# Kernel tuning notes

Hardware: AMD Instinct MI355X
Metric: run time of the kernel (lower is better)

## Reference

```python
import jax, jax.numpy as jnp
from jax import lax
import numpy as np

DIM = 256
HEADS = 8
DIM_HEAD = 32          # must equal W (see rearrange constraint in original code)
INNER = HEADS * DIM_HEAD
FF_INNER = DIM * 4
KH = 8                 # height_top_k (selects over dim_head axis due to axis mislabeling)
KW = 8                 # width_top_k  (selects over spatial H axis)
B, H, W = 8, 256, 32
EPS = 1e-5


def setup_inputs() -> dict:
    key = jax.random.key(0)
    ks = jax.random.split(key, 12)
    def rn(k, shape, fan_in):
        return jax.random.normal(k, shape, dtype=jnp.float32) / np.sqrt(fan_in)
    return {
        "x": jax.random.normal(ks[0], (B, DIM, H, W), dtype=jnp.float32),
        "cln_g": jnp.ones((1, DIM, 1, 1), dtype=jnp.float32),
        "cln_b": jnp.zeros((1, DIM, 1, 1), dtype=jnp.float32),
        "w_qkv": rn(ks[1], (INNER * 3, DIM), DIM),
        "w_out": rn(ks[2], (DIM, INNER), INNER),
        "b_out": jnp.zeros((DIM,), dtype=jnp.float32),
        "w_dw": rn(ks[3], (DIM, 1, 3, 3), 9),
        "b_dw": jnp.zeros((DIM,), dtype=jnp.float32),
        "w_comb": rn(ks[4], (DIM, DIM * 2), DIM * 2),
        "b_comb": jnp.zeros((DIM,), dtype=jnp.float32),
        "w_ff1": rn(ks[5], (FF_INNER, DIM), DIM),
        "b_ff1": jnp.zeros((FF_INNER,), dtype=jnp.float32),
        "w_ffdw": rn(ks[6], (FF_INNER, 1, 3, 3), 9),
        "b_ffdw": jnp.zeros((FF_INNER,), dtype=jnp.float32),
        "w_ff2": rn(ks[7], (DIM, FF_INNER), FF_INNER),
        "b_ff2": jnp.zeros((DIM,), dtype=jnp.float32),
    }


def _conv1x1(x, w, b=None):
    y = jnp.einsum('oc,bchw->bohw', w, x)
    return y if b is None else y + b[None, :, None, None]


def _dwconv3(x, w, b):
    y = lax.conv_general_dilated(x, w, (1, 1), 'SAME',
                                 feature_group_count=x.shape[1],
                                 dimension_numbers=('NCHW', 'OIHW', 'NCHW'))
    return y + b[None, :, None, None]


def _inorm(t):
    # nn.InstanceNorm2d(affine=False): normalize per (b, c) over spatial dims
    m = jnp.mean(t, axis=(2, 3), keepdims=True)
    v = jnp.var(t, axis=(2, 3), keepdims=True)
    return (t - m) / jnp.sqrt(v + EPS)


def _l2n(t):
    # F.normalize(dim=-1): here last axis is spatial W (acts as feature 'd')
    return t / jnp.clip(jnp.linalg.norm(t, axis=-1, keepdims=True), 1e-12)


def reference(x, cln_g, cln_b, w_qkv, w_out, b_out, w_dw, b_dw, w_comb, b_comb,
              w_ff1, b_ff1, w_ffdw, b_ffdw, w_ff2, b_ff2):
    b, c, h, w = x.shape
    # ---- DPSA branch ----
    mean = jnp.mean(x, axis=1, keepdims=True)
    var = jnp.var(x, axis=1, keepdims=True)
    xn = (x - mean) / jnp.sqrt(var + EPS) * cln_g + cln_b
    qkv = _conv1x1(xn, w_qkv)
    q, k, v = jnp.split(qkv, 3, axis=1)
    # '(b h) c x y' layout: axes are (b*heads, dim_head, H, W)
    q, k, v = (t.reshape(b * HEADS, DIM_HEAD, h, w) for t in (q, k, v))
    q, k = _l2n(q), _l2n(k)
    q_probe = q.sum(axis=(1, 2))                       # (bh, W)
    # 'height' selection -> actually over dim_head axis (axis 1)
    sh = jnp.einsum('bd,bhd->bh', q_probe, k.sum(axis=2))
    ih = lax.top_k(sh, KH)[1]                          # (bh, KH)
    k = jnp.take_along_axis(k, ih[:, :, None, None], axis=1)
    v = jnp.take_along_axis(v, ih[:, :, None, None], axis=1)
    # 'width' selection -> actually over spatial H axis (axis 2)
    sw = jnp.einsum('bd,bwd->bw', q_probe, k.sum(axis=1))
    iw = lax.top_k(sw, KW)[1]                          # (bh, KW)
    k = jnp.take_along_axis(k, iw[:, None, :, None], axis=2)
    v = jnp.take_along_axis(v, iw[:, None, :, None], axis=2)
    q2 = q.reshape(b * HEADS, DIM_HEAD * h, w)         # (bh, dh*H, W)
    k2 = k.reshape(b * HEADS, KH * KW, w)
    v2 = v.reshape(b * HEADS, KH * KW, w)
    attn = jax.nn.softmax(jnp.einsum('bid,bjd->bij', q2, k2), axis=-1)
    o = jnp.einsum('bij,bjd->bid', attn, v2)           # (bh, dh*H, W); dh == W
    # rearrange '(b h) (x y) d -> b (h d) x y'
    o = o.reshape(b, HEADS, h, w, w).transpose(0, 1, 4, 2, 3).reshape(b, HEADS * w, h, w)
    attn_branch = _conv1x1(o, w_out, b_out)
    # ---- conv branch + combine ----
    conv_branch = _dwconv3(x, w_dw, b_dw)
    comb = _conv1x1(jnp.concatenate([attn_branch, conv_branch], axis=1), w_comb, b_comb) + x
    # ---- feed-forward ----
    h1 = jax.nn.gelu(_inorm(_conv1x1(comb, w_ff1, b_ff1)), approximate=False)
    h2 = h1 + jax.nn.gelu(_inorm(_dwconv3(h1, w_ffdw, b_ffdw)), approximate=False)
    return _inorm(_conv1x1(h2, w_ff2, b_ff2))
```

## Files before the change

### kernel.cpp

```cpp
#include <hip/hip_runtime.h>
#include <hip/hip_fp16.h>
#include <math.h>

#define B_    8
#define CDIM  256
#define HH    256
#define WW    32
#define PP    8192
#define HEADS 8
#define FFI   1024

typedef _Float16 f16;
typedef _Float16 half8 __attribute__((ext_vector_type(8)));
typedef _Float16 half4 __attribute__((ext_vector_type(4)));
typedef _Float16 f16x2v __attribute__((ext_vector_type(2)));
typedef float f32x4 __attribute__((ext_vector_type(4)));

static const size_t OFF_QPROBE = 16908288;
static const size_t OFF_SH     = 16910336;
static const size_t OFF_IH     = 16912384;
static const size_t OFF_IW     = 16912896;
static const size_t OFF_STM    = 16913408;
static const size_t OFF_STR    = 16921600;
static const size_t OFF_VSEL   = 16929792;
static const size_t OFF_W16    = 17060864;

#define WH_QKV  0
#define WH_OUT  196608
#define WH_COMB 262144
#define WH_FF1  393216
#define WH_FF2  655360

__device__ __forceinline__ float gelu_f(float x) {
  float z = fabsf(x) * 0.70710678118f;
  float t = __builtin_amdgcn_rcpf(1.0f + 0.3275911f * z);
  float poly = t * (0.254829592f +
               t * (-0.284496736f +
               t * (1.421413741f +
               t * (-1.453152027f +
               t * 1.061405429f))));
  float e = 1.0f - poly * __expf(-z * z);
  return 0.5f * x * (1.0f + copysignf(e, x));
}

__global__ __launch_bounds__(256) void k_wcvt(const float* __restrict__ s0,
                                              const float* __restrict__ s1,
                                              const float* __restrict__ s2,
                                              const float* __restrict__ s3,
                                              const float* __restrict__ s4,
                                              f16* __restrict__ dst) {
  int blk = blockIdx.x;
  const float* src; size_t base;
  if (blk < 192)      { src = s0; base = WH_QKV;  }
  else if (blk < 256) { src = s1; base = WH_OUT;  blk -= 192; }
  else if (blk < 384) { src = s2; base = WH_COMB; blk -= 256; }
  else if (blk < 640) { src = s3; base = WH_FF1;  blk -= 384; }
  else                { src = s4; base = WH_FF2;  blk -= 640; }
  int off = blk * 1024 + threadIdx.x * 4;
  float4 v = *(const float4*)(src + off);
  half4 h; h[0] = (f16)v.x; h[1] = (f16)v.y; h[2] = (f16)v.z; h[3] = (f16)v.w;
  *(half4*)(dst + base + off) = h;
}

__global__ __launch_bounds__(256) void k_lnxn(const float* __restrict__ x,
                                              const float* __restrict__ g,
                                              const float* __restrict__ bb,
                                              f16* __restrict__ xn) {
  int idx = blockIdx.x * 256 + threadIdx.x;
  int b = idx >> 13, p = idx & 8191;
  const float* xp = x + (size_t)b * CDIM * PP + p;
  float s = 0.f, s2 = 0.f;
  for (int c = 0; c < CDIM; c++) { float v = xp[(size_t)c * PP]; s += v; s2 += v * v; }
  float m = s * (1.0f / CDIM);
  float var = s2 * (1.0f / CDIM) - m * m;
  float r = rsqrtf(var + 1e-5f);
  f16* xo = xn + (size_t)b * CDIM * PP + p;
  for (int c = 0; c < CDIM; c++)
    xo[(size_t)c * PP] = (f16)((xp[(size_t)c * PP] - m) * r * g[c] + bb[c]);
}

#define MF_STAGE                                                                   \
  int t = threadIdx.x;                                                             \
  int nw_ = gridDim.x * gridDim.y;                     \
  int hb_ = blockIdx.x + gridDim.x * blockIdx.y;                                   \
  int wk_ = (hb_ & 7) * (nw_ >> 3) + (hb_ >> 3);                                   \
  int gy_ = gridDim.y;                                      \
  int sh_ = __ffs(gy_) - 1;                                                        \
  int p0 = (wk_ >> sh_) * 128, m0 = (wk_ & (gy_ - 1)) * 128, z = blockIdx.z;       \
  int lane = t & 63, wave = t >> 6;                                                \
  int wm = (wave >> 1) * 64, wp = (wave & 1) * 64;                                 \
  int col = lane & 15, quad = lane >> 4;                                           \
  f32x4 acc[4][4];                                                                 \
  _Pragma("unroll") for (int i = 0; i < 4; i++)                                    \
  _Pragma("unroll") for (int j = 0; j < 4; j++)                                    \
      acc[i][j] = (f32x4){0.f, 0.f, 0.f, 0.f};                                     \
  int am = t >> 1, ak = (t & 1) * 16;                                              \
  int bp = (t & 15) * 8, bk = (t >> 4) * 2;                                        \
  int erot = t & 7;                                                                \
  const f16* wr0 = W + (size_t)(m0 + am) * K + ak;                                 \
  const f16* br0 = inB + (size_t)bk * PP + p0 + bp;                                \
  half8 w0 = *(const half8*)wr0;                                                   \
  half8 w1 = *(const half8*)(wr0 + 8);                                             \
  half8 r0 = *(const half8*)br0;                                                   \
  half8 r1 = *(const half8*)(br0 + PP);                                            \
  for (int k0 = 0; k0 < K; k0 += 32) {                                             \
    *(half8*)&As[am][ak] = w0;                                                     \
    *(half8*)&As[am][ak + 8] = w1;                                                 \
    _Pragma("unroll") for (int e0 = 0; e0 < 8; e0++) {                             \
      int e = (e0 + erot) & 7;                                                     \
      f16x2v pr2; pr2[0] = r0[e]; pr2[1] = r1[e];                                  \
      *(f16x2v*)&Bs[bp + e][bk] = pr2;                                             \
    }                                                                              \
    __syncthreads();                                                               \
    int kn = (k0 + 32 < K) ? k0 + 32 : k0;  \
    w0 = *(const half8*)(wr0 + kn);                                                \
    w1 = *(const half8*)(wr0 + kn + 8);                                            \
    r0 = *(const half8*)(inB + (size_t)(kn + bk) * PP + p0 + bp);                  \
    r1 = *(const half8*)(inB + (size_t)(kn + bk + 1) * PP + p0 + bp);              \
    half8 af[4], bf[4];                                                            \
    _Pragma("unroll") for (int i = 0; i < 4; i++)                                  \
      af[i] = *(const half8*)&As[wm + i * 16 + col][quad * 8];                     \
    _Pragma("unroll") for (int j = 0; j < 4; j++)                                  \
      bf[j] = *(const half8*)&Bs[wp + j * 16 + col][quad * 8];                     \
    _Pragma("unroll") for (int i = 0; i < 4; i++)                                  \
    _Pragma("unroll") for (int j = 0; j < 4; j++)                                  \
        acc[i][j] = __builtin_amdgcn_mfma_f32_16x16x32_f16(af[i], bf[j],           \
                                                           acc[i][j], 0, 0, 0);    \
    __syncthreads();                                                               \
  }

__global__ __launch_bounds__(256) void k_mf(const f16* __restrict__ W,
                                            const f16* __restrict__ In, size_t inZ,
                                            f16* __restrict__ OutH,
                                            float* __restrict__ OutF, size_t outZ,
                                            const float* __restrict__ bias,
                                            const float* __restrict__ resid, size_t residZ,
                                            int K) {
  __shared__ f16 As[128][40];
  __shared__ f16 Bs[128][40];
  const f16* inB = In + (size_t)blockIdx.z * inZ;
  MF_STAGE
#pragma unroll
  for (int i = 0; i < 4; i++) {
    int mb = m0 + wm + i * 16 + quad * 4;
#pragma unroll
    for (int r = 0; r < 4; r++) {
      int m = mb + r;
      float bs = bias ? bias[m] : 0.f;
#pragma unroll
      for (int j = 0; j < 4; j++) {
        int p = p0 + wp + j * 16 + col;
        float v = acc[i][j][r] + bs;
        size_t off = (size_t)z * outZ + (size_t)m * PP + p;
        if (resid) v += resid[(size_t)z * residZ + (size_t)m * PP + p];
        if (OutF) OutF[off] = v;
        else OutH[off] = (f16)v;
      }
    }
  }
}

__global__ __launch_bounds__(256) void k_mf_qk(const f16* __restrict__ W,
                                               const f16* __restrict__ In, size_t inZ,
                                               f16* __restrict__ qkO, int K) {
  __shared__ f16 As[128][40];
  __shared__ f16 Bs[128][40];
  const f16* inB = In + (size_t)blockIdx.z * inZ;
  MF_STAGE
#pragma unroll
  for (int i = 0; i < 4; i++) {
    int mb = m0 + wm + i * 16 + quad * 4;
#pragma unroll
    for (int r = 0; r < 4; r++) {
      int m = mb + r;
      size_t base = (size_t)z * 512 * PP + (size_t)m * PP;
#pragma unroll
      for (int jp = 0; jp < 2; jp++) {
        float a0 = acc[i][2 * jp][r], a1 = acc[i][2 * jp + 1][r];
        float ss = a0 * a0 + a1 * a1;
        ss += __shfl_xor(ss, 1);
        ss += __shfl_xor(ss, 2);
        ss += __shfl_xor(ss, 4);
        ss += __shfl_xor(ss, 8);
        float inv = 1.0f / fmaxf(sqrtf(ss), 1e-12f);
        int pa = p0 + wp + 2 * jp * 16 + col;
        qkO[base + pa] = (f16)(a0 * inv);
        qkO[base + pa + 16] = (f16)(a1 * inv);
      }
    }
  }
}

__global__ __launch_bounds__(256) void k_probe(const f16* __restrict__ qk,
                                               float* __restrict__ qprobe,
                                               float* __restrict__ sh) {
  __shared__ float red[64][32];
  __shared__ float qp[32];
  __shared__ float ksum[32][32];
  int bh = blockIdx.x, b = bh >> 3, hd = bh & 7;
  int t = threadIdx.x;
  const f16* qb = qk + ((size_t)(b * 512 + hd * 32)) * PP;
  {
    int g = t >> 2, wq = (t & 3) * 8;
    float s[8];
#pragma unroll
    for (int e = 0; e < 8; e++) s[e] = 0.f;
    for (int it = 0; it < 128; it++) {
      int row = g * 128 + it;
      half8 v = *(const half8*)(qb + (size_t)(row >> 8) * PP + (row & 255) * 32 + wq);
#pragma unroll
      for (int e = 0; e < 8; e++) s[e] += (float)v[e];
    }
#pragma unroll
    for (int e = 0; e < 8; e++) red[g][wq + e] = s[e];
  }
  __syncthreads();
  if (t < 32) {
    float a = 0.f;
    for (int g = 0; g < 64; g++) a += red[g][t];
    qp[t] = a;
    qprobe[bh * 32 + t] = a;
  }
  const f16* kb = qk + ((size_t)(b * 512 + 256 + hd * 32)) * PP;
  {
    int d = t >> 3, wq = (t & 7) * 4;
    float s[4] = {0.f, 0.f, 0.f, 0.f};
    for (int h = 0; h < 256; h++) {
      half4 v = *(const half4*)(kb + (size_t)d * PP + h * 32 + wq);
#pragma unroll
      for (int e = 0; e < 4; e++) s[e] += (float)v[e];
    }
#pragma unroll
    for (int e = 0; e < 4; e++) ksum[d][wq + e] = s[e];
  }
  __syncthreads();
  if (t < 32) {
    float a = 0.f;
    for (int w = 0; w < 32; w++) a += qp[w] * ksum[t][w];
    sh[bh * 32 + t] = a;
  }
}

__global__ __launch_bounds__(64) void k_topk_h(const float* __restrict__ sh, int* __restrict__ ih) {
  int bh = blockIdx.x;
  if (threadIdx.x != 0) return;
  float v[32];
#pragma unroll
  for (int i = 0; i < 32; i++) v[i] = sh[bh * 32 + i];
  for (int s = 0; s < 8; s++) {
    int bi = 0; float bv = v[0];
#pragma unroll
    for (int i = 1; i < 32; i++) { if (v[i] > bv) { bv = v[i]; bi = i; } }
    ih[bh * 8 + s] = bi;
    v[bi] = -3.4e38f;
  }
}

__global__ __launch_bounds__(256) void k_sw_topk(const f16* __restrict__ qk,
                                                 const float* __restrict__ qprobe,
                                                 const int* __restrict__ ih,
                                                 int* __restrict__ iw) {
  __shared__ float qp[32];
  __shared__ float sw[256];
  __shared__ int ihs[8];
  int bh = blockIdx.x, b = bh >> 3, hd = bh & 7;
  int t = threadIdx.x;
  if (t < 32) qp[t] = qprobe[bh * 32 + t];
  if (t < 8) ihs[t] = ih[bh * 8 + t];
  __syncthreads();
  const f16* kb = qk + ((size_t)(b * 512 + 256 + hd * 32)) * PP;
  float s = 0.f;
  for (int a = 0; a < 8; a++) {
    const f16* kd = kb + (size_t)ihs[a] * PP + t * 32;
#pragma unroll
    for (int w = 0; w < 32; w++) s += qp[w] * (float)kd[w];
  }
  sw[t] = s;
  __syncthreads();
  if (t == 0) {
    for (int sel = 0; sel < 8; sel++) {
      int bi = 0; float bv = sw[0];
      for (int i = 1; i < 256; i++) { if (sw[i] > bv) { bv = sw[i]; bi = i; } }
      iw[bh * 8 + sel] = bi;
      sw[bi] = -3.4e38f;
    }
  }
}

__global__ __launch_bounds__(256) void k_vsel2(const f16* __restrict__ xn,
                                               const f16* __restrict__ W16,
                                               const int* __restrict__ ih,
                                               const int* __restrict__ iw,
                                               float* __restrict__ vsel) {
  __shared__ f16 xg[64][264];
  __shared__ float wrow[8][64];
  __shared__ int ihs[8], iws8[8];
  int bh = blockIdx.x, b = bh >> 3, hd = bh & 7;
  int t = threadIdx.x;
  if (t < 8) { ihs[t] = ih[bh * 8 + t]; iws8[t] = iw[bh * 8 + t]; }
  __syncthreads();
  float acc[8];
#pragma unroll
  for (int a = 0; a < 8; a++) acc[a] = 0.f;
  for (int c0 = 0; c0 < 256; c0 += 64) {
    for (int rep = 0; rep < 2; rep++) {
      int cc = rep * 32 + (t >> 3);
      int seg = t & 7;
#pragma unroll
      for (int u = 0; u < 4; u++) {
        int h8 = seg * 4 + u;
        int bi = h8 >> 2, wq = (h8 & 3) * 8;
        half8 v = *(const half8*)(xn + ((size_t)(b * 256 + c0 + cc)) * PP + iws8[bi] * 32 + wq);
        *(half8*)&xg[cc][h8 * 8] = v;
      }
    }
    for (int rep = 0; rep < 2; rep++) {
      int idx = t + rep * 256;
      int a = idx >> 6, cc = idx & 63;
      wrow[a][cc] = (float)W16[(size_t)(512 + hd * 32 + ihs[a]) * 256 + c0 + cc];
    }
    __syncthreads();
    for (int cc = 0; cc < 64; cc++) {
      float xv = (float)xg[cc][t];
#pragma unroll
      for (int a = 0; a < 8; a++) acc[a] += wrow[a][cc] * xv;
    }
    __syncthreads();
  }
  int bi = t >> 5, w = t & 31;
#pragma unroll
  for (int a = 0; a < 8; a++)
    vsel[((size_t)bh * 64 + a * 8 + bi) * 32 + w] = acc[a];
}

__global__ __launch_bounds__(256) void k_attn_mf(const f16* __restrict__ qk,
                                                 const float* __restrict__ vsel,
                                                 const int* __restrict__ ih,
                                                 const int* __restrict__ iw,
                                                 f16* __restrict__ o_r) {
  __shared__ f16 Ks[64][40];
  __shared__ f16 Vt[32][72];
  __shared__ f16 Ps[4][32][72];
  __shared__ f16 Os[32][136];
  __shared__ int ihs[8], iws8[8];
  int bh = blockIdx.y, b = bh >> 3, hd = bh & 7;
  int t = threadIdx.x;
  if (t < 8) { ihs[t] = ih[bh * 8 + t]; iws8[t] = iw[bh * 8 + t]; }
  __syncthreads();
  {
    int j = t >> 2, wc = (t & 3) * 8;
    const f16* kb = qk + ((size_t)(b * 512 + 256 + hd * 32 + ihs[j >> 3])) * PP
                    + iws8[j & 7] * 32 + wc;
    *(half8*)&Ks[j][wc] = *(const half8*)kb;
  }
  for (int rep = 0; rep < 2; rep++) {
    int idx = t + rep * 256;
    int j = idx >> 3, w4 = (idx & 7) * 4;
    float4 v = *(const float4*)(vsel + ((size_t)bh * 64 + j) * 32 + w4);
    Vt[w4 + 0][j] = (f16)v.x; Vt[w4 + 1][j] = (f16)v.y;
    Vt[w4 + 2][j] = (f16)v.z; Vt[w4 + 3][j] = (f16)v.w;
  }
  __syncthreads();
  int wv = t >> 6, lane = t & 63, col = lane & 15, quad = lane >> 4;
  int i0 = blockIdx.x * 128;
  int dq = i0 >> 8;
  int hb = (i0 & 255) + wv * 32;
  const f16* qbase = qk + ((size_t)(b * 512 + hd * 32 + dq)) * PP;
  f32x4 sacc[2][4];
#pragma unroll
  for (int i = 0; i < 2; i++)
#pragma unroll
    for (int j = 0; j < 4; j++) sacc[i][j] = (f32x4){0.f, 0.f, 0.f, 0.f};
#pragma unroll
  for (int mt = 0; mt < 2; mt++) {
    half8 af = *(const half8*)(qbase + (size_t)(hb + mt * 16 + col) * 32 + quad * 8);
#pragma unroll
    for (int nt = 0; nt < 4; nt++) {
      half8 bf = *(const half8*)&Ks[nt * 16 + col][quad * 8];
      sacc[mt][nt] = __builtin_amdgcn_mfma_f32_16x16x32_f16(af, bf, sacc[mt][nt], 0, 0, 0);
    }
  }
#pragma unroll
  for (int mt = 0; mt < 2; mt++) {
#pragma unroll
    for (int r = 0; r < 4; r++) {
      float s0 = sacc[mt][0][r], s1 = sacc[mt][1][r], s2 = sacc[mt][2][r], s3 = sacc[mt][3][r];
      float mx = fmaxf(fmaxf(s0, s1), fmaxf(s2, s3));
      mx = fmaxf(mx, __shfl_xor(mx, 1));
      mx = fmaxf(mx, __shfl_xor(mx, 2));
      mx = fmaxf(mx, __shfl_xor(mx, 4));
      mx = fmaxf(mx, __shfl_xor(mx, 8));
      float e0 = __expf(s0 - mx), e1 = __expf(s1 - mx), e2 = __expf(s2 - mx), e3 = __expf(s3 - mx);
      float l = e0 + e1 + e2 + e3;
      l += __shfl_xor(l, 1);
      l += __shfl_xor(l, 2);
      l += __shfl_xor(l, 4);
      l += __shfl_xor(l, 8);
      float inv = 1.0f / l;
      int row = mt * 16 + quad * 4 + r;
      Ps[wv][row][0 * 16 + col] = (f16)(e0 * inv);
      Ps[wv][row][1 * 16 + col] = (f16)(e1 * inv);
      Ps[wv][row][2 * 16 + col] = (f16)(e2 * inv);
      Ps[wv][row][3 * 16 + col] = (f16)(e3 * inv);
    }
  }
  __syncthreads();
  f32x4 oacc[2][2];
#pragma unroll
  for (int i = 0; i < 2; i++)
#pragma unroll
    for (int j = 0; j < 2; j++) oacc[i][j] = (f32x4){0.f, 0.f, 0.f, 0.f};
#pragma unroll
  for (int kk = 0; kk < 2; kk++) {
    half8 ap[2], bv[2];
#pragma unroll
    for (int mt = 0; mt < 2; mt++) ap[mt] = *(const half8*)&Ps[wv][mt * 16 + col][kk * 32 + quad * 8];
#pragma unroll
    for (int wn = 0; wn < 2; wn++) bv[wn] = *(const half8*)&Vt[wn * 16 + col][kk * 32 + quad * 8];
#pragma unroll
    for (int mt = 0; mt < 2; mt++)
#pragma unroll
      for (int wn = 0; wn < 2; wn++)
        oacc[mt][wn] = __builtin_amdgcn_mfma_f32_16x16x32_f16(ap[mt], bv[wn], oacc[mt][wn], 0, 0, 0);
  }
#pragma unroll
  for (int mt = 0; mt < 2; mt++)
#pragma unroll
    for (int wn = 0; wn < 2; wn++)
#pragma unroll
      for (int r = 0; r < 4; r++)
        Os[wn * 16 + col][wv * 32 + mt * 16 + quad * 4 + r] = (f16)oacc[mt][wn][r];
  __syncthreads();
  {
    int dd = t >> 3, seg = t & 7;
#pragma unroll
    for (int u = 0; u < 2; u++) {
      int io = (seg * 2 + u) * 8;
      *(half8*)(o_r + ((size_t)(b * 256 + hd * 32 + dd)) * PP + i0 + io) = *(const half8*)&Os[dd][io];
    }
  }
}

__global__ __launch_bounds__(256) void k_dw(const float* __restrict__ in,
                                            const float* __restrict__ wdw,
                                            const float* __restrict__ bdw,
                                            f16* __restrict__ out) {
  int bc = blockIdx.x;
  int b = bc >> 8, c = bc & 255;
  int p = blockIdx.y * 256 + threadIdx.x;
  int x0 = p >> 5, y0 = p & 31;
  const float* ip = in + (size_t)bc * PP;
  const float* wp = wdw + c * 9;
  float s = bdw[c];
#pragma unroll
  for (int i = 0; i < 3; i++) {
    int xx = x0 + i - 1;
    if (xx < 0 || xx >= HH) continue;
#pragma unroll
    for (int j = 0; j < 3; j++) {
      int yy = y0 + j - 1;
      if (yy < 0 || yy >= WW) continue;
      s += wp[i * 3 + j] * ip[xx * 32 + yy];
    }
  }
  out[((size_t)(b * 512 + 256 + c)) * PP + p] = (f16)s;
}

__global__ __launch_bounds__(256) void k_ff_fused(const f16* __restrict__ h1,
                                                  const float* __restrict__ wdw,
                                                  const float* __restrict__ bdw,
                                                  f16* __restrict__ h2) {
  __shared__ float gbuf[256 * 33];
  __shared__ float redA[8], redB[8];
  int c = blockIdx.x, zz = blockIdx.y;
  int t = threadIdx.x;
  int wv = t >> 6, lane = t & 63;
  const f16* hp = h1 + ((size_t)zz * FFI + c) * PP;
  f16* out = h2 + ((size_t)zz * FFI + c) * PP;

  float v[32];
  float s = 0.f, s2 = 0.f;
#pragma unroll
  for (int u = 0; u < 4; u++) {
    half8 h = *(const half8*)(hp + (u * 256 + t) * 8);
#pragma unroll
    for (int e = 0; e < 8; e++) { float f = (float)h[e]; v[u * 8 + e] = f; s += f; s2 += f * f; }
  }
#pragma unroll
  for (int o = 32; o; o >>= 1) { s += __shfl_xor(s, o); s2 += __shfl_xor(s2, o); }
  if (lane == 0) { redA[wv] = s; redA[4 + wv] = s2; }
  __syncthreads();
  float m = (redA[0] + redA[1] + redA[2] + redA[3]) * (1.0f / PP);
  float s2a = (redA[4] + redA[5] + redA[6] + redA[7]) * (1.0f / PP);
  float r = rsqrtf(s2a - m * m + 1e-5f);

#pragma unroll
  for (int u = 0; u < 4; u++) {
    int base = (u * 256 + t) * 8;
    int row = base >> 5, colb = base & 31;
#pragma unroll
    for (int e = 0; e < 8; e++)
      gbuf[row * 33 + colb + e] = gelu_f((v[u * 8 + e] - m) * r);
  }
  __syncthreads();

  float wf[9];
#pragma unroll
  for (int i = 0; i < 9; i++) wf[i] = wdw[c * 9 + i];
  float bd = bdw[c];
  float g0[32];
#pragma unroll
  for (int y = 0; y < 32; y++) g0[y] = gbuf[t * 33 + y];
  const float* up = (t > 0) ? &gbuf[(t - 1) * 33] : nullptr;
  const float* dn = (t < 255) ? &gbuf[(t + 1) * 33] : nullptr;
  float d[32];
  float sd = 0.f, sd2 = 0.f;
#pragma unroll
  for (int y = 0; y < 32; y++) {
    float um1 = 0.f, u0 = 0.f, up1 = 0.f;
    float dm1 = 0.f, d0 = 0.f, dp1 = 0.f;
    if (up) { u0 = up[y]; if (y > 0) um1 = up[y - 1]; if (y < 31) up1 = up[y + 1]; }
    if (dn) { d0 = dn[y]; if (y > 0) dm1 = dn[y - 1]; if (y < 31) dp1 = dn[y + 1]; }
    float a = bd + wf[1] * u0 + wf[4] * g0[y] + wf[7] * d0;
    if (y > 0)  a += wf[0] * um1 + wf[3] * g0[y - 1] + wf[6] * dm1;
    if (y < 31) a += wf[2] * up1 + wf[5] * g0[y + 1] + wf[8] * dp1;
    d[y] = a; sd += a; sd2 += a * a;
  }
#pragma unroll
  for (int o = 32; o; o >>= 1) { sd += __shfl_xor(sd, o); sd2 += __shfl_xor(sd2, o); }
  if (lane == 0) { redB[wv] = sd; redB[4 + wv] = sd2; }
  __syncthreads();
  float dm = (redB[0] + redB[1] + redB[2] + redB[3]) * (1.0f / PP);
  float dv = (redB[4] + redB[5] + redB[6] + redB[7]) * (1.0f / PP);
  float dr = rsqrtf(dv - dm * dm + 1e-5f);

#pragma unroll
  for (int y = 0; y < 32; y++)
    gbuf[t * 33 + y] = g0[y] + gelu_f((d[y] - dm) * dr);
  __syncthreads();

#pragma unroll
  for (int u = 0; u < 4; u++) {
    int base = (u * 256 + t) * 8;
    int row = base >> 5, colb = base & 31;
    half8 h;
#pragma unroll
    for (int e = 0; e < 8; e++) h[e] = (f16)gbuf[row * 33 + colb + e];
    *(half8*)(out + base) = h;
  }
}

__global__ __launch_bounds__(256) void k_istats(const float* __restrict__ in,
                                                float* __restrict__ stm,
                                                float* __restrict__ str) {
  __shared__ float ss[256], ss2[256];
  int row = blockIdx.x, t = threadIdx.x;
  const float* p = in + (size_t)row * PP;
  float s = 0.f, s2 = 0.f;
  for (int i = t; i < PP; i += 256) { float v = p[i]; s += v; s2 += v * v; }
  ss[t] = s; ss2[t] = s2;
  __syncthreads();
  for (int off = 128; off; off >>= 1) {
    if (t < off) { ss[t] += ss[t + off]; ss2[t] += ss2[t + off]; }
    __syncthreads();
  }
  if (t == 0) {
    float m = ss[0] * (1.0f / PP);
    float var = ss2[0] * (1.0f / PP) - m * m;
    stm[row] = m;
    str[row] = rsqrtf(var + 1e-5f);
  }
}

__global__ __launch_bounds__(256) void k_napply(float* __restrict__ io,
                                                const float* __restrict__ stm,
                                                const float* __restrict__ str) {
  size_t idx = (size_t)blockIdx.x * 256 + threadIdx.x;
  int row = (int)(idx >> 13);
  io[idx] = (io[idx] - stm[row]) * str[row];
}

extern "C" void kernel_launch(void* const* d_in, const int* in_sizes, int n_in,
                              void* d_out, int out_size, void* d_ws, size_t ws_size,
                              hipStream_t stream) {
  const float* x      = (const float*)d_in[0];
  const float* cln_g  = (const float*)d_in[1];
  const float* cln_b  = (const float*)d_in[2];
  const float* w_qkv  = (const float*)d_in[3];
  const float* w_out  = (const float*)d_in[4];
  const float* b_out  = (const float*)d_in[5];
  const float* w_dw   = (const float*)d_in[6];
  const float* b_dw   = (const float*)d_in[7];
  const float* w_comb = (const float*)d_in[8];
  const float* b_comb = (const float*)d_in[9];
  const float* w_ff1  = (const float*)d_in[10];
  const float* b_ff1  = (const float*)d_in[11];
  const float* w_ffdw = (const float*)d_in[12];
  const float* b_ffdw = (const float*)d_in[13];
  const float* w_ff2  = (const float*)d_in[14];
  const float* b_ff2  = (const float*)d_in[15];
  float* outF = (float*)d_out;

  float* ws = (float*)d_ws;
  f16* qk    = (f16*)ws;
  f16* bv512 = (f16*)ws;
  f16* h1    = (f16*)ws;
  f16* h2    = (f16*)ws + 16777216;
  f16* xn    = (f16*)d_out;
  f16* o_r   = (f16*)d_out;
  f16* combT = (f16*)d_out;
  float* qprobe = ws + OFF_QPROBE;
  float* sh     = ws + OFF_SH;
  int*   ih     = (int*)(ws + OFF_IH);
  int*   iw     = (int*)(ws + OFF_IW);
  float* stm    = ws + OFF_STM;
  float* str    = ws + OFF_STR;
  float* vsel   = ws + OFF_VSEL;
  f16*   W16    = (f16*)(ws + OFF_W16);

  hipLaunchKernelGGL(k_wcvt, dim3(896), dim3(256), 0, stream,
                     w_qkv, w_out, w_comb, w_ff1, w_ff2, W16);
  hipLaunchKernelGGL(k_lnxn, dim3(256), dim3(256), 0, stream, x, cln_g, cln_b, xn);
  hipLaunchKernelGGL(k_mf_qk, dim3(64, 4, 8), dim3(256), 0, stream,
                     W16 + WH_QKV, xn, (size_t)CDIM * PP, qk, 256);
  hipLaunchKernelGGL(k_probe, dim3(64), dim3(256), 0, stream, qk, qprobe, sh);
  hipLaunchKernelGGL(k_topk_h, dim3(64), dim3(64), 0, stream, sh, ih);
  hipLaunchKernelGGL(k_sw_topk, dim3(64), dim3(256), 0, stream, qk, qprobe, ih, iw);
  hipLaunchKernelGGL(k_vsel2, dim3(64), dim3(256), 0, stream, xn, W16 + WH_QKV, ih, iw, vsel);
  hipLaunchKernelGGL(k_attn_mf, dim3(64, 64), dim3(256), 0, stream, qk, vsel, ih, iw, o_r);
  hipLaunchKernelGGL(k_mf, dim3(64, 2, 8), dim3(256), 0, stream,
                     W16 + WH_OUT, o_r, (size_t)CDIM * PP, bv512, (float*)nullptr, (size_t)512 * PP,
                     b_out, (const float*)nullptr, (size_t)0, 256);
  hipLaunchKernelGGL(k_dw, dim3(2048, 32), dim3(256), 0, stream, x, w_dw, b_dw, bv512);
  hipLaunchKernelGGL(k_mf, dim3(64, 2, 8), dim3(256), 0, stream,
                     W16 + WH_COMB, bv512, (size_t)512 * PP, combT, (float*)nullptr, (size_t)CDIM * PP,
                     b_comb, x, (size_t)CDIM * PP, 512);
  for (int b = 6; b >= 0; b -= 2) {
    hipLaunchKernelGGL(k_mf, dim3(64, 8, 2), dim3(256), 0, stream,
                       W16 + WH_FF1, combT + (size_t)b * CDIM * PP, (size_t)CDIM * PP,
                       h1, (float*)nullptr, (size_t)FFI * PP, b_ff1,
                       (const float*)nullptr, (size_t)0, 256);
    hipLaunchKernelGGL(k_ff_fused, dim3(FFI, 2), dim3(256), 0, stream,
                       h1, w_ffdw, b_ffdw, h2);
    hipLaunchKernelGGL(k_mf, dim3(64, 2, 2), dim3(256), 0, stream,
                       W16 + WH_FF2, h2, (size_t)FFI * PP,
                       (f16*)nullptr, outF + (size_t)b * CDIM * PP, (size_t)CDIM * PP,
                       b_ff2, (const float*)nullptr, (size_t)0, 1024);
  }
  hipLaunchKernelGGL(k_istats, dim3(2048), dim3(256), 0, stream, outF, stm, str);
  hipLaunchKernelGGL(k_napply, dim3(65536), dim3(256), 0, stream, outF, stm, str);
}
```

Baseline: 981.6 us.

## Use 256x128 MFMA GEMM tiles with LDS-staged vectorized f16 epilogue

Adds a GEMM variant whose block computes 256 output rows instead of 128, reusing each loaded B tile for two M sub-tiles and halving the number of blocks. The epilogue now stages results through shared memory and writes them as 16-byte half8 stores instead of scattered 2-byte stores. This applies to the QK projection, the out-projection, the combine conv and FF1. The cost is twice the accumulator registers, larger LDS and fewer blocks, which may lower occupancy and grid parallelism.

```diff
diff --git a/kernel.cpp b/kernel.cpp
--- a/kernel.cpp
+++ b/kernel.cpp
@@ -81,10 +81,10 @@
 
 #define MF_STAGE                                                                   \
   int t = threadIdx.x;                                                             \
-  int nw_ = gridDim.x * gridDim.y;                     \
+  int nw_ = gridDim.x * gridDim.y;                                                 \
   int hb_ = blockIdx.x + gridDim.x * blockIdx.y;                                   \
   int wk_ = (hb_ & 7) * (nw_ >> 3) + (hb_ >> 3);                                   \
-  int gy_ = gridDim.y;                                      \
+  int gy_ = gridDim.y;                                                             \
   int sh_ = __ffs(gy_) - 1;                                                        \
   int p0 = (wk_ >> sh_) * 128, m0 = (wk_ & (gy_ - 1)) * 128, z = blockIdx.z;       \
   int lane = t & 63, wave = t >> 6;                                                \
@@ -112,7 +112,7 @@
       *(f16x2v*)&Bs[bp + e][bk] = pr2;                                             \
     }                                                                              \
     __syncthreads();                                                               \
-    int kn = (k0 + 32 < K) ? k0 + 32 : k0;  \
+    int kn = (k0 + 32 < K) ? k0 + 32 : k0;                                         \
     w0 = *(const half8*)(wr0 + kn);                                                \
     w1 = *(const half8*)(wr0 + kn + 8);                                            \
     r0 = *(const half8*)(inB + (size_t)(kn + bk) * PP + p0 + bp);                  \
@@ -160,32 +160,156 @@
   }
 }
 
-__global__ __launch_bounds__(256) void k_mf_qk(const f16* __restrict__ W,
-                                               const f16* __restrict__ In, size_t inZ,
-                                               f16* __restrict__ qkO, int K) {
-  __shared__ f16 As[128][40];
+#define MF_STAGE2                                                                  \
+  int t = threadIdx.x;                                                             \
+  int nw_ = gridDim.x * gridDim.y;                                                 \
+  int hb_ = blockIdx.x + gridDim.x * blockIdx.y;                                   \
+  int wk_ = (hb_ & 7) * (nw_ >> 3) + (hb_ >> 3);                                   \
+  int gy_ = gridDim.y;                                                             \
+  int sh_ = __ffs(gy_) - 1;                                                        \
+  int p0 = (wk_ >> sh_) * 128, m0 = (wk_ & (gy_ - 1)) * 256, z = blockIdx.z;       \
+  int lane = t & 63, wave = t >> 6;                                                \
+  int wm = (wave >> 1) * 64, wp = (wave & 1) * 64;                                 \
+  int col = lane & 15, quad = lane >> 4;                                           \
+  f32x4 acc[2][4][4];                                                              \
+  _Pragma("unroll") for (int mt = 0; mt < 2; mt++)                                 \
+  _Pragma("unroll") for (int i = 0; i < 4; i++)                                    \
+  _Pragma("unroll") for (int j = 0; j < 4; j++)                                    \
+      acc[mt][i][j] = (f32x4){0.f, 0.f, 0.f, 0.f};                                 \
+  int am = t >> 1, ak = (t & 1) * 16;                                              \
+  int bp = (t & 15) * 8, bk = (t >> 4) * 2;                                        \
+  int erot = t & 7;                                                                \
+  const f16* wr0 = W + (size_t)(m0 + am) * K + ak;                                 \
+  const f16* wr1 = wr0 + (size_t)128 * K;                                          \
+  const f16* br0 = inB + (size_t)bk * PP + p0 + bp;                                \
+  half8 w0 = *(const half8*)wr0;                                                   \
+  half8 w1 = *(const half8*)(wr0 + 8);                                             \
+  half8 w2 = *(const half8*)wr1;                                                   \
+  half8 w3 = *(const half8*)(wr1 + 8);                                             \
+  half8 r0 = *(const half8*)br0;                                                   \
+  half8 r1 = *(const half8*)(br0 + PP);                                            \
+  for (int k0 = 0; k0 < K; k0 += 32) {                                             \
+    *(half8*)&As[am][ak] = w0;                                                     \
+    *(half8*)&As[am][ak + 8] = w1;                                                 \
+    *(half8*)&As[128 + am][ak] = w2;                                               \
+    *(half8*)&As[128 + am][ak + 8] = w3;                                           \
+    _Pragma("unroll") for (int e0 = 0; e0 < 8; e0++) {                             \
+      int e = (e0 + erot) & 7;                                                     \
+      f16x2v pr2; pr2[0] = r0[e]; pr2[1] = r1[e];                                  \
+      *(f16x2v*)&Bs[bp + e][bk] = pr2;                                             \
+    }                                                                              \
+    __syncthreads();                                                               \
+    int kn = (k0 + 32 < K) ? k0 + 32 : k0;                                         \
+    w0 = *(const half8*)(wr0 + kn);                                                \
+    w1 = *(const half8*)(wr0 + kn + 8);                                            \
+    w2 = *(const half8*)(wr1 + kn);                                                \
+    w3 = *(const half8*)(wr1 + kn + 8);                                            \
+    r0 = *(const half8*)(inB + (size_t)(kn + bk) * PP + p0 + bp);                  \
+    r1 = *(const half8*)(inB + (size_t)(kn + bk + 1) * PP + p0 + bp);              \
+    half8 bf[4];                                                                   \
+    _Pragma("unroll") for (int j = 0; j < 4; j++)                                  \
+      bf[j] = *(const half8*)&Bs[wp + j * 16 + col][quad * 8];                     \
+    _Pragma("unroll") for (int mt = 0; mt < 2; mt++) {                             \
+      half8 af[4];                                                                 \
+      _Pragma("unroll") for (int i = 0; i < 4; i++)                                \
+        af[i] = *(const half8*)&As[mt * 128 + wm + i * 16 + col][quad * 8];        \
+      _Pragma("unroll") for (int i = 0; i < 4; i++)                                \
+      _Pragma("unroll") for (int j = 0; j < 4; j++)                                \
+          acc[mt][i][j] = __builtin_amdgcn_mfma_f32_16x16x32_f16(af[i], bf[j],     \
+                                                         acc[mt][i][j], 0, 0, 0); \
+    }                                                                              \
+    __syncthreads();                                                               \
+  }
+
+__global__ __launch_bounds__(256) void k_mf2(const f16* __restrict__ W,
+                                             const f16* __restrict__ In, size_t inZ,
+                                             f16* __restrict__ OutH, size_t outZ,
+                                             const float* __restrict__ bias,
+                                             const float* __restrict__ resid, size_t residZ,
+                                             int K) {
+  __shared__ f16 As[256][40];
   __shared__ f16 Bs[128][40];
   const f16* inB = In + (size_t)blockIdx.z * inZ;
-  MF_STAGE
-#pragma unroll
-  for (int i = 0; i < 4; i++) {
-    int mb = m0 + wm + i * 16 + quad * 4;
-#pragma unroll
-    for (int r = 0; r < 4; r++) {
-      int m = mb + r;
-      size_t base = (size_t)z * 512 * PP + (size_t)m * PP;
-#pragma unroll
-      for (int jp = 0; jp < 2; jp++) {
-        float a0 = acc[i][2 * jp][r], a1 = acc[i][2 * jp + 1][r];
-        float ss = a0 * a0 + a1 * a1;
-        ss += __shfl_xor(ss, 1);
-        ss += __shfl_xor(ss, 2);
-        ss += __shfl_xor(ss, 4);
-        ss += __shfl_xor(ss, 8);
-        float inv = 1.0f / fmaxf(sqrtf(ss), 1e-12f);
-        int pa = p0 + wp + 2 * jp * 16 + col;
-        qkO[base + pa] = (f16)(a0 * inv);
-        qkO[base + pa + 16] = (f16)(a1 * inv);
+  MF_STAGE2
+  f16 (*ebuf)[136] = (f16(*)[136])&As[0][0];
+#pragma unroll
+  for (int mt = 0; mt < 2; mt++) {
+#pragma unroll
+    for (int half = 0; half < 2; half++) {
+      __syncthreads();
+      if (wm == half * 64) {
+#pragma unroll
+        for (int i = 0; i < 4; i++) {
+#pragma unroll
+          for (int r = 0; r < 4; r++) {
+            int lr = i * 16 + quad * 4 + r;
+            int m = m0 + mt * 128 + half * 64 + lr;
+            float bs = bias ? bias[m] : 0.f;
+#pragma unroll
+            for (int j = 0; j < 4; j++) {
+              float v = acc[mt][i][j][r] + bs;
+              if (resid)
+                v += resid[(size_t)z * residZ + (size_t)m * PP + p0 + wp + j * 16 + col];
+              ebuf[lr][wp + j * 16 + col] = (f16)v;
+            }
+          }
+        }
+      }
+      __syncthreads();
+#pragma unroll
+      for (int u = 0; u < 4; u++) {
+        int idx = u * 256 + t;
+        int row = idx >> 4, seg = idx & 15;
+        int m = m0 + mt * 128 + half * 64 + row;
+        *(half8*)(OutH + (size_t)z * outZ + (size_t)m * PP + p0 + seg * 8) =
+            *(const half8*)&ebuf[row][seg * 8];
+      }
+    }
+  }
+}
+
+__global__ __launch_bounds__(256) void k_mf_qk2(const f16* __restrict__ W,
+                                                const f16* __restrict__ In, size_t inZ,
+                                                f16* __restrict__ qkO, int K) {
+  __shared__ f16 As[256][40];
+  __shared__ f16 Bs[128][40];
+  const f16* inB = In + (size_t)blockIdx.z * inZ;
+  MF_STAGE2
+  f16 (*ebuf)[136] = (f16(*)[136])&As[0][0];
+#pragma unroll
+  for (int mt = 0; mt < 2; mt++) {
+#pragma unroll
+    for (int half = 0; half < 2; half++) {
+      __syncthreads();
+      if (wm == half * 64) {
+#pragma unroll
+        for (int i = 0; i < 4; i++) {
+#pragma unroll
+          for (int r = 0; r < 4; r++) {
+            int lr = i * 16 + quad * 4 + r;
+#pragma unroll
+            for (int jp = 0; jp < 2; jp++) {
+              float a0 = acc[mt][i][2 * jp][r], a1 = acc[mt][i][2 * jp + 1][r];
+              float ss = a0 * a0 + a1 * a1;
+              ss += __shfl_xor(ss, 1);
+              ss += __shfl_xor(ss, 2);
+              ss += __shfl_xor(ss, 4);
+              ss += __shfl_xor(ss, 8);
+              float inv = 1.0f / fmaxf(sqrtf(ss), 1e-12f);
+              ebuf[lr][wp + 2 * jp * 16 + col] = (f16)(a0 * inv);
+              ebuf[lr][wp + 2 * jp * 16 + col + 16] = (f16)(a1 * inv);
+            }
+          }
+        }
+      }
+      __syncthreads();
+#pragma unroll
+      for (int u = 0; u < 4; u++) {
+        int idx = u * 256 + t;
+        int row = idx >> 4, seg = idx & 15;
+        int m = m0 + mt * 128 + half * 64 + row;
+        *(half8*)(qkO + (size_t)z * 512 * PP + (size_t)m * PP + p0 + seg * 8) =
+            *(const half8*)&ebuf[row][seg * 8];
       }
     }
   }
@@ -621,24 +745,24 @@
   hipLaunchKernelGGL(k_wcvt, dim3(896), dim3(256), 0, stream,
                      w_qkv, w_out, w_comb, w_ff1, w_ff2, W16);
   hipLaunchKernelGGL(k_lnxn, dim3(256), dim3(256), 0, stream, x, cln_g, cln_b, xn);
-  hipLaunchKernelGGL(k_mf_qk, dim3(64, 4, 8), dim3(256), 0, stream,
+  hipLaunchKernelGGL(k_mf_qk2, dim3(64, 2, 8), dim3(256), 0, stream,
                      W16 + WH_QKV, xn, (size_t)CDIM * PP, qk, 256);
   hipLaunchKernelGGL(k_probe, dim3(64), dim3(256), 0, stream, qk, qprobe, sh);
   hipLaunchKernelGGL(k_topk_h, dim3(64), dim3(64), 0, stream, sh, ih);
   hipLaunchKernelGGL(k_sw_topk, dim3(64), dim3(256), 0, stream, qk, qprobe, ih, iw);
   hipLaunchKernelGGL(k_vsel2, dim3(64), dim3(256), 0, stream, xn, W16 + WH_QKV, ih, iw, vsel);
   hipLaunchKernelGGL(k_attn_mf, dim3(64, 64), dim3(256), 0, stream, qk, vsel, ih, iw, o_r);
-  hipLaunchKernelGGL(k_mf, dim3(64, 2, 8), dim3(256), 0, stream,
-                     W16 + WH_OUT, o_r, (size_t)CDIM * PP, bv512, (float*)nullptr, (size_t)512 * PP,
+  hipLaunchKernelGGL(k_mf2, dim3(64, 1, 8), dim3(256), 0, stream,
+                     W16 + WH_OUT, o_r, (size_t)CDIM * PP, bv512, (size_t)512 * PP,
                      b_out, (const float*)nullptr, (size_t)0, 256);
   hipLaunchKernelGGL(k_dw, dim3(2048, 32), dim3(256), 0, stream, x, w_dw, b_dw, bv512);
-  hipLaunchKernelGGL(k_mf, dim3(64, 2, 8), dim3(256), 0, stream,
-                     W16 + WH_COMB, bv512, (size_t)512 * PP, combT, (float*)nullptr, (size_t)CDIM * PP,
+  hipLaunchKernelGGL(k_mf2, dim3(64, 1, 8), dim3(256), 0, stream,
+                     W16 + WH_COMB, bv512, (size_t)512 * PP, combT, (size_t)CDIM * PP,
                      b_comb, x, (size_t)CDIM * PP, 512);
   for (int b = 6; b >= 0; b -= 2) {
-    hipLaunchKernelGGL(k_mf, dim3(64, 8, 2), dim3(256), 0, stream,
+    hipLaunchKernelGGL(k_mf2, dim3(64, 4, 2), dim3(256), 0, stream,
                        W16 + WH_FF1, combT + (size_t)b * CDIM * PP, (size_t)CDIM * PP,
-                       h1, (float*)nullptr, (size_t)FFI * PP, b_ff1,
+                       h1, (size_t)FFI * PP, b_ff1,
                        (const float*)nullptr, (size_t)0, 256);
     hipLaunchKernelGGL(k_ff_fused, dim3(FFI, 2), dim3(256), 0, stream,
                        h1, w_ffdw, b_ffdw, h2);
```

Measured after the change: 1.222 ms. +24.5%, slower.

## Use 512-thread MFMA GEMM with 256x128 tiles for 1x1 convs

Applied to the files above, without the earlier changes.

Adds k_mf8 and k_mf_qk8, which compute a 256-row by 128-pixel output tile per block with 8 waves, and grids halved in the M dimension. They replace the 128x128 GEMMs for qkv, out-projection, combine and FF1. The goal is to reuse each staged input (B) tile across twice as many weight rows, cutting global and LDS traffic for activations. In exchange, each block uses more LDS, only half the threads load B, and there are half as many blocks, which may lower occupancy or load balance.

```diff
diff --git a/kernel.cpp b/kernel.cpp
--- a/kernel.cpp
+++ b/kernel.cpp
@@ -81,10 +81,10 @@
 
 #define MF_STAGE                                                                   \
   int t = threadIdx.x;                                                             \
-  int nw_ = gridDim.x * gridDim.y;                     \
+  int nw_ = gridDim.x * gridDim.y;                                                 \
   int hb_ = blockIdx.x + gridDim.x * blockIdx.y;                                   \
   int wk_ = (hb_ & 7) * (nw_ >> 3) + (hb_ >> 3);                                   \
-  int gy_ = gridDim.y;                                      \
+  int gy_ = gridDim.y;                                                             \
   int sh_ = __ffs(gy_) - 1;                                                        \
   int p0 = (wk_ >> sh_) * 128, m0 = (wk_ & (gy_ - 1)) * 128, z = blockIdx.z;       \
   int lane = t & 63, wave = t >> 6;                                                \
@@ -112,7 +112,7 @@
       *(f16x2v*)&Bs[bp + e][bk] = pr2;                                             \
     }                                                                              \
     __syncthreads();                                                               \
-    int kn = (k0 + 32 < K) ? k0 + 32 : k0;  \
+    int kn = (k0 + 32 < K) ? k0 + 32 : k0;                                         \
     w0 = *(const half8*)(wr0 + kn);                                                \
     w1 = *(const half8*)(wr0 + kn + 8);                                            \
     r0 = *(const half8*)(inB + (size_t)(kn + bk) * PP + p0 + bp);                  \
@@ -160,13 +160,96 @@
   }
 }
 
-__global__ __launch_bounds__(256) void k_mf_qk(const f16* __restrict__ W,
-                                               const f16* __restrict__ In, size_t inZ,
-                                               f16* __restrict__ qkO, int K) {
-  __shared__ f16 As[128][40];
+#define MF_STAGE8                                                                  \
+  int t = threadIdx.x;                                                             \
+  int nw_ = gridDim.x * gridDim.y;                                                 \
+  int hb_ = blockIdx.x + gridDim.x * blockIdx.y;                                   \
+  int wk_ = (hb_ & 7) * (nw_ >> 3) + (hb_ >> 3);                                   \
+  int gy_ = gridDim.y;                                                             \
+  int sh_ = __ffs(gy_) - 1;                                                        \
+  int p0 = (wk_ >> sh_) * 128, m0 = (wk_ & (gy_ - 1)) * 256, z = blockIdx.z;       \
+  int lane = t & 63, wave = t >> 6;                                                \
+  int wm = (wave >> 1) * 64, wp = (wave & 1) * 64;                                 \
+  int col = lane & 15, quad = lane >> 4;                                           \
+  f32x4 acc[4][4];                                                                 \
+  _Pragma("unroll") for (int i = 0; i < 4; i++)                                    \
+  _Pragma("unroll") for (int j = 0; j < 4; j++)                                    \
+      acc[i][j] = (f32x4){0.f, 0.f, 0.f, 0.f};                                     \
+  int am = t >> 1, ak = (t & 1) * 16;                                              \
+  int bp = (t & 15) * 8, bk = (t >> 4) * 2;         \
+  int erot = t & 7;                                                                \
+  const f16* wr0 = W + (size_t)(m0 + am) * K + ak;                                 \
+  const f16* br0 = inB + (size_t)(bk & 31) * PP + p0 + bp;                         \
+  half8 w0 = *(const half8*)wr0;                                                   \
+  half8 w1 = *(const half8*)(wr0 + 8);                                             \
+  half8 r0 = {}, r1 = {};                                                          \
+  if (t < 256) { r0 = *(const half8*)br0; r1 = *(const half8*)(br0 + PP); }        \
+  for (int k0 = 0; k0 < K; k0 += 32) {                                             \
+    *(half8*)&As[am][ak] = w0;                                                     \
+    *(half8*)&As[am][ak + 8] = w1;                                                 \
+    if (t < 256) {                                                                 \
+      _Pragma("unroll") for (int e0 = 0; e0 < 8; e0++) {                           \
+        int e = (e0 + erot) & 7;                                                   \
+        f16x2v pr2; pr2[0] = r0[e]; pr2[1] = r1[e];                                \
+        *(f16x2v*)&Bs[bp + e][bk] = pr2;                                           \
+      }                                                                            \
+    }                                                                              \
+    __syncthreads();                                                               \
+    int kn = (k0 + 32 < K) ? k0 + 32 : k0;                                         \
+    w0 = *(const half8*)(wr0 + kn);                                                \
+    w1 = *(const half8*)(wr0 + kn + 8);                                            \
+    if (t < 256) {                                                                 \
+      r0 = *(const half8*)(inB + (size_t)(kn + bk) * PP + p0 + bp);                \
+      r1 = *(const half8*)(inB + (size_t)(kn + bk + 1) * PP + p0 + bp);            \
+    }                                                                              \
+    half8 af[4], bf[4];                                                            \
+    _Pragma("unroll") for (int i = 0; i < 4; i++)                                  \
+      af[i] = *(const half8*)&As[wm + i * 16 + col][quad * 8];                     \
+    _Pragma("unroll") for (int j = 0; j < 4; j++)                                  \
+      bf[j] = *(const half8*)&Bs[wp + j * 16 + col][quad * 8];                     \
+    _Pragma("unroll") for (int i = 0; i < 4; i++)                                  \
+    _Pragma("unroll") for (int j = 0; j < 4; j++)                                  \
+        acc[i][j] = __builtin_amdgcn_mfma_f32_16x16x32_f16(af[i], bf[j],           \
+                                                           acc[i][j], 0, 0, 0);    \
+    __syncthreads();                                                               \
+  }
+
+__global__ __launch_bounds__(512) void k_mf8(const f16* __restrict__ W,
+                                             const f16* __restrict__ In, size_t inZ,
+                                             f16* __restrict__ OutH, size_t outZ,
+                                             const float* __restrict__ bias,
+                                             const float* __restrict__ resid, size_t residZ,
+                                             int K) {
+  __shared__ f16 As[256][40];
   __shared__ f16 Bs[128][40];
   const f16* inB = In + (size_t)blockIdx.z * inZ;
-  MF_STAGE
+  MF_STAGE8
+#pragma unroll
+  for (int i = 0; i < 4; i++) {
+    int mb = m0 + wm * 4 / 4 + i * 16 + quad * 4;
+#pragma unroll
+    for (int r = 0; r < 4; r++) {
+      int m = mb + r;
+      float bs = bias ? bias[m] : 0.f;
+#pragma unroll
+      for (int j = 0; j < 4; j++) {
+        int p = p0 + wp + j * 16 + col;
+        float v = acc[i][j][r] + bs;
+        size_t off = (size_t)z * outZ + (size_t)m * PP + p;
+        if (resid) v += resid[(size_t)z * residZ + (size_t)m * PP + p];
+        OutH[off] = (f16)v;
+      }
+    }
+  }
+}
+
+__global__ __launch_bounds__(512) void k_mf_qk8(const f16* __restrict__ W,
+                                                const f16* __restrict__ In, size_t inZ,
+                                                f16* __restrict__ qkO, int K) {
+  __shared__ f16 As[256][40];
+  __shared__ f16 Bs[128][40];
+  const f16* inB = In + (size_t)blockIdx.z * inZ;
+  MF_STAGE8
 #pragma unroll
   for (int i = 0; i < 4; i++) {
     int mb = m0 + wm + i * 16 + quad * 4;
@@ -621,24 +704,24 @@
   hipLaunchKernelGGL(k_wcvt, dim3(896), dim3(256), 0, stream,
                      w_qkv, w_out, w_comb, w_ff1, w_ff2, W16);
   hipLaunchKernelGGL(k_lnxn, dim3(256), dim3(256), 0, stream, x, cln_g, cln_b, xn);
-  hipLaunchKernelGGL(k_mf_qk, dim3(64, 4, 8), dim3(256), 0, stream,
+  hipLaunchKernelGGL(k_mf_qk8, dim3(64, 2, 8), dim3(512), 0, stream,
                      W16 + WH_QKV, xn, (size_t)CDIM * PP, qk, 256);
   hipLaunchKernelGGL(k_probe, dim3(64), dim3(256), 0, stream, qk, qprobe, sh);
   hipLaunchKernelGGL(k_topk_h, dim3(64), dim3(64), 0, stream, sh, ih);
   hipLaunchKernelGGL(k_sw_topk, dim3(64), dim3(256), 0, stream, qk, qprobe, ih, iw);
   hipLaunchKernelGGL(k_vsel2, dim3(64), dim3(256), 0, stream, xn, W16 + WH_QKV, ih, iw, vsel);
   hipLaunchKernelGGL(k_attn_mf, dim3(64, 64), dim3(256), 0, stream, qk, vsel, ih, iw, o_r);
-  hipLaunchKernelGGL(k_mf, dim3(64, 2, 8), dim3(256), 0, stream,
-                     W16 + WH_OUT, o_r, (size_t)CDIM * PP, bv512, (float*)nullptr, (size_t)512 * PP,
+  hipLaunchKernelGGL(k_mf8, dim3(64, 1, 8), dim3(512), 0, stream,
+                     W16 + WH_OUT, o_r, (size_t)CDIM * PP, bv512, (size_t)512 * PP,
                      b_out, (const float*)nullptr, (size_t)0, 256);
   hipLaunchKernelGGL(k_dw, dim3(2048, 32), dim3(256), 0, stream, x, w_dw, b_dw, bv512);
-  hipLaunchKernelGGL(k_mf, dim3(64, 2, 8), dim3(256), 0, stream,
-                     W16 + WH_COMB, bv512, (size_t)512 * PP, combT, (float*)nullptr, (size_t)CDIM * PP,
+  hipLaunchKernelGGL(k_mf8, dim3(64, 1, 8), dim3(512), 0, stream,
+                     W16 + WH_COMB, bv512, (size_t)512 * PP, combT, (size_t)CDIM * PP,
                      b_comb, x, (size_t)CDIM * PP, 512);
   for (int b = 6; b >= 0; b -= 2) {
-    hipLaunchKernelGGL(k_mf, dim3(64, 8, 2), dim3(256), 0, stream,
+    hipLaunchKernelGGL(k_mf8, dim3(64, 4, 2), dim3(512), 0, stream,
                        W16 + WH_FF1, combT + (size_t)b * CDIM * PP, (size_t)CDIM * PP,
-                       h1, (float*)nullptr, (size_t)FFI * PP, b_ff1,
+                       h1, (size_t)FFI * PP, b_ff1,
                        (const float*)nullptr, (size_t)0, 256);
     hipLaunchKernelGGL(k_ff_fused, dim3(FFI, 2), dim3(256), 0, stream,
                        h1, w_ffdw, b_ffdw, h2);
```

Result: no change. 983.9 us (+0.2%).
